# Kernel optimization log

Hardware: AMD Instinct MI355X
Metric: run time of the kernel (lower is better)

## Reference

```python
import jax, jax.numpy as jnp
import numpy as np

B, S, D, E, K, F = 2, 1024, 1024, 8, 2, 2048


def setup_inputs() -> dict:
    key = jax.random.key(0)
    k0, k1, k2, k3 = jax.random.split(key, 4)
    x = jax.random.normal(k0, (B, S, D), dtype=jnp.float32)
    gate_w = (jax.random.normal(k1, (E, D), dtype=jnp.float32) * 0.02)  # nn.init.normal_(std=0.02)
    # nn.Linear default init ~ U(-1/sqrt(fan_in), 1/sqrt(fan_in)); use same scale
    w1 = jax.random.uniform(k2, (E, F, D), dtype=jnp.float32, minval=-1.0, maxval=1.0) / np.float32(np.sqrt(D))
    w2 = jax.random.uniform(k3, (E, D, F), dtype=jnp.float32, minval=-1.0, maxval=1.0) / np.float32(np.sqrt(F))
    norm_w = jnp.ones((D,), dtype=jnp.float32)
    scale = jnp.full((1,), -4.0, dtype=jnp.float32)
    return {"x": x, "gate_w": gate_w, "w1": w1, "w2": w2, "norm_w": norm_w, "scale": scale}


def reference(x, gate_w, w1, w2, norm_w, scale):
    b, s, d = x.shape
    e = gate_w.shape[0]
    t = b * s
    eps = jnp.finfo(x.dtype).eps  # torch RMSNorm eps=None -> dtype eps
    # RMSNorm
    xn = x * jax.lax.rsqrt(jnp.mean(x * x, axis=-1, keepdims=True) + eps) * norm_w
    xf = xn.reshape(t, d)
    # router
    logits = xf @ gate_w.T                       # [T, E]
    prob = jax.nn.softmax(logits, axis=-1)
    topk_w, topk_e = jax.lax.top_k(prob, K)      # [T, K]
    topk_w = topk_w / jnp.clip(jnp.sum(topk_w, axis=-1, keepdims=True), 1e-6)
    # dense combine weights [T, E]: sum of slot weights routed to each expert
    combine = jnp.sum(jax.nn.one_hot(topk_e, e, dtype=xf.dtype) * topk_w[..., None], axis=1)
    # all-expert FFN, weighted combine (same math as the gather/index_add loop)
    h = jax.nn.silu(jnp.einsum('td,efd->tef', xf, w1))   # [T, E, F]
    out = jnp.einsum('tef,edf,te->td', h, w2, combine)    # [T, D]
    # load-balance aux loss (Switch eq.4), f_e from top-1 slot, detached
    f_e = jnp.mean(jax.nn.one_hot(topk_e[:, 0], e, dtype=prob.dtype), axis=0)
    lb_loss = e * jnp.sum(jax.lax.stop_gradient(f_e) * jnp.mean(prob, axis=0))
    sc = jax.nn.sigmoid(scale)[0]
    return (x + sc * out.reshape(b, s, d), lb_loss)
```

## Files before the change

kernel.cpp:

```cpp
#include <hip/hip_runtime.h>
#include <stdint.h>

#define T_TOK 2048
#define DD 1024
#define EE 8
#define FF 2048
#define NSLOT 4096
#define SLOTPAD 4224
#define CVT_BLOCKS 6144

typedef __attribute__((ext_vector_type(8))) __bf16 bf16x8;
typedef __attribute__((ext_vector_type(4))) float floatx4;

__device__ __forceinline__ unsigned short f2bf(float f){
  union { float f; unsigned u; } v; v.f = f;
  unsigned r = v.u + 0x7fffu + ((v.u >> 16) & 1u);
  return (unsigned short)(r >> 16);
}

__global__ __launch_bounds__(256) void k_front(
    const float* __restrict__ x, const float* __restrict__ gw,
    const float* __restrict__ nw,
    const float* __restrict__ w1, const float* __restrict__ w2,
    unsigned short* __restrict__ xn,
    int* __restrict__ topk_id, float* __restrict__ topk_w,
    float* __restrict__ probbuf,
    unsigned short* __restrict__ w1b, unsigned short* __restrict__ w2b)
{
  const int tid = threadIdx.x;
  if (blockIdx.x >= T_TOK){
    const int n4 = EE * FF * DD / 4;
    int i = (blockIdx.x - T_TOK) * 256 + tid;
    const int stride = CVT_BLOCKS * 256;
    for (; i < 2 * n4; i += stride){
      const int j = (i < n4) ? i : i - n4;
      const float4 v = (i < n4) ? ((const float4*)w1)[j] : ((const float4*)w2)[j];
      ushort4 o; o.x = f2bf(v.x); o.y = f2bf(v.y); o.z = f2bf(v.z); o.w = f2bf(v.w);
      if (i < n4) ((ushort4*)w1b)[j] = o; else ((ushort4*)w2b)[j] = o;
    }
    return;
  }
  const int t = blockIdx.x;
  const float4 xv = ((const float4*)(x + (size_t)t * DD))[tid];
  float ss = xv.x*xv.x + xv.y*xv.y + xv.z*xv.z + xv.w*xv.w;
  #pragma unroll
  for (int o = 32; o > 0; o >>= 1) ss += __shfl_down(ss, o);
  __shared__ float s_ss[4];
  __shared__ float s_p[4][8];
  if ((tid & 63) == 0) s_ss[tid >> 6] = ss;
  __syncthreads();
  const float tot = s_ss[0] + s_ss[1] + s_ss[2] + s_ss[3];
  const float inv = rsqrtf(tot * (1.0f / DD) + 1.1920929e-7f);
  const float4 nv = ((const float4*)nw)[tid];
  float4 xnv;
  xnv.x = xv.x*inv*nv.x; xnv.y = xv.y*inv*nv.y;
  xnv.z = xv.z*inv*nv.z; xnv.w = xv.w*inv*nv.w;
  ushort4 bv; bv.x = f2bf(xnv.x); bv.y = f2bf(xnv.y); bv.z = f2bf(xnv.z); bv.w = f2bf(xnv.w);
  ((ushort4*)(xn + (size_t)t * DD))[tid] = bv;
  float p[8];
  #pragma unroll
  for (int e = 0; e < 8; e++){
    const float4 g = ((const float4*)(gw + e * DD))[tid];
    p[e] = xnv.x*g.x + xnv.y*g.y + xnv.z*g.z + xnv.w*g.w;
  }
  #pragma unroll
  for (int e = 0; e < 8; e++){
    #pragma unroll
    for (int o = 32; o > 0; o >>= 1) p[e] += __shfl_down(p[e], o);
  }
  if ((tid & 63) == 0){
    #pragma unroll
    for (int e = 0; e < 8; e++) s_p[tid >> 6][e] = p[e];
  }
  __syncthreads();
  if (tid == 0){
    float lg[8], pr[8];
    #pragma unroll
    for (int e = 0; e < 8; e++) lg[e] = s_p[0][e] + s_p[1][e] + s_p[2][e] + s_p[3][e];
    float mx = lg[0];
    for (int e = 1; e < 8; e++) mx = fmaxf(mx, lg[e]);
    float sum = 0.f;
    for (int e = 0; e < 8; e++){ pr[e] = __expf(lg[e] - mx); sum += pr[e]; }
    const float is = 1.f / sum;
    for (int e = 0; e < 8; e++) pr[e] *= is;
    #pragma unroll
    for (int e = 0; e < 8; e++) probbuf[t * 8 + e] = pr[e];
    int e1 = 0;
    for (int e = 1; e < 8; e++) if (pr[e] > pr[e1]) e1 = e;
    int e2 = (e1 == 0) ? 1 : 0;
    for (int e = 0; e < 8; e++) if (e != e1 && e != e2 && pr[e] > pr[e2]) e2 = e;
    const float wsum = fmaxf(pr[e1] + pr[e2], 1e-6f);
    topk_id[2*t] = e1; topk_id[2*t+1] = e2;
    topk_w[2*t] = pr[e1] / wsum; topk_w[2*t+1] = pr[e2] / wsum;
  }
}

__global__ __launch_bounds__(256) void k_stats(
    const int* __restrict__ topk_id, const float* __restrict__ topk_w,
    const float* __restrict__ probbuf,
    int* __restrict__ counts, int* __restrict__ bases,
    int* __restrict__ slots_of, int* __restrict__ tok_of,
    float* __restrict__ slot_w,
    float* __restrict__ lb_out)
{
  const int tid = threadIdx.x;
  __shared__ int s_scan[256][8];
  __shared__ int s_base[8];

  int ids[16];
  int lc[8] = {}, lc1[8] = {};
  float lsp[8] = {};
  #pragma unroll
  for (int j = 0; j < 8; j++){
    const int t = tid * 8 + j;
    const int e1 = topk_id[2*t], e2 = topk_id[2*t+1];
    ids[2*j] = e1; ids[2*j+1] = e2;
    lc[e1]++; lc[e2]++; lc1[e1]++;
    const float4 p0 = ((const float4*)(probbuf + t * 8))[0];
    const float4 p1 = ((const float4*)(probbuf + t * 8))[1];
    lsp[0] += p0.x; lsp[1] += p0.y; lsp[2] += p0.z; lsp[3] += p0.w;
    lsp[4] += p1.x; lsp[5] += p1.y; lsp[6] += p1.z; lsp[7] += p1.w;
  }
  #pragma unroll
  for (int e = 0; e < 8; e++) s_scan[tid][e] = lc[e];
  __syncthreads();
  for (int off = 1; off < 256; off <<= 1){
    int v[8];
    if (tid >= off){
      #pragma unroll
      for (int e = 0; e < 8; e++) v[e] = s_scan[tid - off][e];
    }
    __syncthreads();
    if (tid >= off){
      #pragma unroll
      for (int e = 0; e < 8; e++) s_scan[tid][e] += v[e];
    }
    __syncthreads();
  }
  int   rc1[8]; float rsp[8];
  #pragma unroll
  for (int e = 0; e < 8; e++){ rc1[e] = lc1[e]; rsp[e] = lsp[e]; }
  #pragma unroll
  for (int e = 0; e < 8; e++){
    #pragma unroll
    for (int o = 32; o > 0; o >>= 1){
      rc1[e] += __shfl_down(rc1[e], o);
      rsp[e] += __shfl_down(rsp[e], o);
    }
  }
  __shared__ int   s_c1[4][8];
  __shared__ float s_sp[4][8];
  if ((tid & 63) == 0){
    const int w = tid >> 6;
    #pragma unroll
    for (int e = 0; e < 8; e++){ s_c1[w][e] = rc1[e]; s_sp[w][e] = rsp[e]; }
  }
  __syncthreads();
  if (tid == 0){
    int b = 0; float lb = 0.f;
    for (int e = 0; e < 8; e++){
      const int tot = s_scan[255][e];
      counts[e] = tot; bases[e] = b; s_base[e] = b; b += tot;
      const int   c1 = s_c1[0][e] + s_c1[1][e] + s_c1[2][e] + s_c1[3][e];
      const float sp = s_sp[0][e] + s_sp[1][e] + s_sp[2][e] + s_sp[3][e];
      lb += (float)c1 * sp;
    }
    lb_out[0] = 8.f * lb * (1.f / ((float)T_TOK * (float)T_TOK));
  }
  __syncthreads();
  int rank[8];
  #pragma unroll
  for (int e = 0; e < 8; e++) rank[e] = s_scan[tid][e] - lc[e];
  #pragma unroll
  for (int j = 0; j < 8; j++){
    const int t = tid * 8 + j;
    #pragma unroll
    for (int k = 0; k < 2; k++){
      const int e = ids[2*j + k];
      const int slot = s_base[e] + rank[e]++;
      slots_of[2*t + k] = slot;
      tok_of[slot] = t;
      slot_w[slot] = topk_w[2*t + k];
    }
  }
}

template<int KDIM, int NDIM, int MODE>
__global__ __launch_bounds__(256) void k_gemm(
    const unsigned short* __restrict__ Ag,
    const unsigned short* __restrict__ Bw,
    const int* __restrict__ counts, const int* __restrict__ bases,
    const int* __restrict__ tok_of,
    const float* __restrict__ slot_w,
    void* __restrict__ Cout)
{
  constexpr int NT = NDIM / 128;
  const int e  = blockIdx.x & 7;
  const int g  = blockIdx.x >> 3;
  const int mt = g / NT;
  const int nt = g - mt * NT;
  const int M = counts[e];
  if (mt * 128 >= M) return;
  const int sbase = bases[e];

  __shared__ __align__(16) unsigned short As[128 * 32];
  __shared__ __align__(16) unsigned short Bs[128 * 32];

  const int tid = threadIdx.x;
  const int l = tid & 63;
  const int w = tid >> 6;
  const int wm = (w >> 1) * 64, wn = (w & 1) * 64;
  const int lrow = l & 15, lq = l >> 4;

  const unsigned short* arow[2];
  int kcs[2];
  #pragma unroll
  for (int i = 0; i < 2; i++){
    const int c = tid + i * 256;
    const int row = c >> 2, q = c & 3;
    kcs[i] = ((q - (row >> 1)) & 3) * 8;
    if (MODE == 0){
      const int slot = min(sbase + mt * 128 + row, NSLOT - 1);
      arow[i] = Ag + (size_t)tok_of[slot] * KDIM;
    } else {
      arow[i] = Ag + (size_t)(sbase + mt * 128 + row) * KDIM;
    }
  }
  const unsigned short* B0 = Bw + (size_t)e * NDIM * KDIM + (size_t)(nt * 128) * KDIM;

  floatx4 acc[4][4] = {};

  for (int k0 = 0; k0 < KDIM; k0 += 32){
    #pragma unroll
    for (int i = 0; i < 2; i++){
      const int c = tid + i * 256;
      const int row = c >> 2;
      const unsigned short* ga = arow[i] + k0 + kcs[i];
      const unsigned short* gb = B0 + (size_t)row * KDIM + k0 + kcs[i];
      __builtin_amdgcn_global_load_lds(
          (__attribute__((address_space(1))) unsigned int*)ga,
          (__attribute__((address_space(3))) unsigned int*)(As + c * 8), 16, 0, 0);
      __builtin_amdgcn_global_load_lds(
          (__attribute__((address_space(1))) unsigned int*)gb,
          (__attribute__((address_space(3))) unsigned int*)(Bs + c * 8), 16, 0, 0);
    }
    __syncthreads();
    bf16x8 af[4], bfv[4];
    #pragma unroll
    for (int mi = 0; mi < 4; mi++){
      const int row = wm + mi * 16 + lrow;
      const int p = (lq + (row >> 1)) & 3;
      af[mi] = *(const bf16x8*)(As + row * 32 + p * 8);
    }
    #pragma unroll
    for (int ni = 0; ni < 4; ni++){
      const int row = wn + ni * 16 + lrow;
      const int p = (lq + (row >> 1)) & 3;
      bfv[ni] = *(const bf16x8*)(Bs + row * 32 + p * 8);
    }
    #pragma unroll
    for (int mi = 0; mi < 4; mi++)
      #pragma unroll
      for (int ni = 0; ni < 4; ni++)
        acc[mi][ni] = __builtin_amdgcn_mfma_f32_16x16x32_bf16(af[mi], bfv[ni], acc[mi][ni], 0, 0, 0);
    __syncthreads();
  }

  const int rb = lq * 4;
  #pragma unroll
  for (int mi = 0; mi < 4; mi++){
    #pragma unroll
    for (int r = 0; r < 4; r++){
      const int row = mt * 128 + wm + mi * 16 + rb + r;
      if (row < M){
        #pragma unroll
        for (int ni = 0; ni < 4; ni++){
          const int col = nt * 128 + wn + ni * 16 + (l & 15);
          const float v = acc[mi][ni][r];
          if (MODE == 0){
            const float s = v / (1.f + __expf(-v));
            ((unsigned short*)Cout)[(size_t)(sbase + row) * NDIM + col] = f2bf(s);
          } else {
            const float wgt = slot_w[sbase + row];
            ((float*)Cout)[(size_t)(sbase + row) * NDIM + col] = v * wgt;
          }
        }
      }
    }
  }
}

__global__ __launch_bounds__(256) void k_combine(
    const float* __restrict__ x, const float* __restrict__ Og,
    const int* __restrict__ slots_of, const float* __restrict__ scale,
    float* __restrict__ out)
{
  const int i = blockIdx.x * 256 + threadIdx.x;
  const int t = i >> 8;
  const int j = i & 255;
  const int s0 = slots_of[2*t], s1 = slots_of[2*t+1];
  const float4 a = ((const float4*)(Og + (size_t)s0 * DD))[j];
  const float4 b = ((const float4*)(Og + (size_t)s1 * DD))[j];
  const float4 xv = ((const float4*)x)[i];
  const float sc = 1.f / (1.f + __expf(-scale[0]));
  float4 o;
  o.x = xv.x + sc * (a.x + b.x);
  o.y = xv.y + sc * (a.y + b.y);
  o.z = xv.z + sc * (a.z + b.z);
  o.w = xv.w + sc * (a.w + b.w);
  ((float4*)out)[i] = o;
}

extern "C" void kernel_launch(void* const* d_in, const int* in_sizes, int n_in,
                              void* d_out, int out_size, void* d_ws, size_t ws_size,
                              hipStream_t stream)
{
  const float* x     = (const float*)d_in[0];
  const float* gw    = (const float*)d_in[1];
  const float* w1    = (const float*)d_in[2];
  const float* w2    = (const float*)d_in[3];
  const float* nw    = (const float*)d_in[4];
  const float* scale = (const float*)d_in[5];
  float* out = (float*)d_out;

  char* ws = (char*)d_ws;
  int*   counts  = (int*)(ws + 0);
  int*   bases   = (int*)(ws + 64);
  int*   topk_id = (int*)(ws + 1024);
  float* topk_w  = (float*)(ws + 20480);
  int*   slots_of= (int*)(ws + 40960);
  float* slot_w  = (float*)(ws + 61440);
  int*   tok_of  = (int*)(ws + 81920);
  float* probbuf = (float*)(ws + 102400);
  unsigned short* xn  = (unsigned short*)(ws + 262144);
  unsigned short* Hg  = xn + (size_t)T_TOK * DD;
  float*          Og  = (float*)(Hg + (size_t)SLOTPAD * FF);
  unsigned short* w1b = (unsigned short*)(Og + (size_t)SLOTPAD * DD);
  unsigned short* w2b = w1b + (size_t)EE * FF * DD;

  k_front<<<T_TOK + CVT_BLOCKS, 256, 0, stream>>>(x, gw, nw, w1, w2, xn,
                                                  topk_id, topk_w, probbuf, w1b, w2b);
  k_stats<<<1, 256, 0, stream>>>(topk_id, topk_w, probbuf, counts, bases,
                                 slots_of, tok_of, slot_w, out + (size_t)T_TOK * DD);
  k_gemm<1024, 2048, 0><<<EE * 16 * (FF/128), 256, 0, stream>>>(xn, w1b, counts, bases, tok_of, nullptr, Hg);
  k_gemm<2048, 1024, 1><<<EE * 16 * (DD/128), 256, 0, stream>>>(Hg, w2b, counts, bases, nullptr, slot_w, Og);
  k_combine<<<T_TOK * DD / 4 / 256, 256, 0, stream>>>(x, Og, slots_of, scale, out);
}
```

Before: 274.5 us.

## Convert fp32 expert weights to bf16 inside GEMM loads instead of separate pass

Drops the separate weight-conversion pass over both fp32 expert weight tensors. The GEMMs now read fp32 weights directly, convert them to bf16 in registers and store them to LDS, which removes a full write and re-read of the bf16 weight copies. The second GEMM's output is also stored as bf16, halving the combine kernel's traffic, and the grid order is changed so M-tiles vary fastest for weight reuse in cache. The trade-off is twice the global bytes per weight tile inside the GEMM, synchronous register-path loads instead of direct-to-LDS loads, and lower output precision.

```diff
diff --git a/kernel.cpp b/kernel.cpp
--- a/kernel.cpp
+++ b/kernel.cpp
@@ -7,40 +7,28 @@
 #define FF 2048
 #define NSLOT 4096
 #define SLOTPAD 4224
-#define CVT_BLOCKS 6144
 
 typedef __attribute__((ext_vector_type(8))) __bf16 bf16x8;
 typedef __attribute__((ext_vector_type(4))) float floatx4;
+typedef __attribute__((ext_vector_type(8))) unsigned short ushort8;
 
 __device__ __forceinline__ unsigned short f2bf(float f){
   union { float f; unsigned u; } v; v.f = f;
   unsigned r = v.u + 0x7fffu + ((v.u >> 16) & 1u);
   return (unsigned short)(r >> 16);
 }
-
-__global__ __launch_bounds__(256) void k_front(
+__device__ __forceinline__ float bf2f(unsigned short h){
+  union { unsigned u; float f; } v; v.u = (unsigned)h << 16; return v.f;
+}
+
+__global__ __launch_bounds__(256) void k_rms_router(
     const float* __restrict__ x, const float* __restrict__ gw,
     const float* __restrict__ nw,
-    const float* __restrict__ w1, const float* __restrict__ w2,
     unsigned short* __restrict__ xn,
     int* __restrict__ topk_id, float* __restrict__ topk_w,
-    float* __restrict__ probbuf,
-    unsigned short* __restrict__ w1b, unsigned short* __restrict__ w2b)
-{
-  const int tid = threadIdx.x;
-  if (blockIdx.x >= T_TOK){
-    const int n4 = EE * FF * DD / 4;
-    int i = (blockIdx.x - T_TOK) * 256 + tid;
-    const int stride = CVT_BLOCKS * 256;
-    for (; i < 2 * n4; i += stride){
-      const int j = (i < n4) ? i : i - n4;
-      const float4 v = (i < n4) ? ((const float4*)w1)[j] : ((const float4*)w2)[j];
-      ushort4 o; o.x = f2bf(v.x); o.y = f2bf(v.y); o.z = f2bf(v.z); o.w = f2bf(v.w);
-      if (i < n4) ((ushort4*)w1b)[j] = o; else ((ushort4*)w2b)[j] = o;
-    }
-    return;
-  }
-  const int t = blockIdx.x;
+    float* __restrict__ probbuf)
+{
+  const int t = blockIdx.x, tid = threadIdx.x;
   const float4 xv = ((const float4*)(x + (size_t)t * DD))[tid];
   float ss = xv.x*xv.x + xv.y*xv.y + xv.z*xv.z + xv.w*xv.w;
   #pragma unroll
@@ -188,17 +176,17 @@
 template<int KDIM, int NDIM, int MODE>
 __global__ __launch_bounds__(256) void k_gemm(
     const unsigned short* __restrict__ Ag,
-    const unsigned short* __restrict__ Bw,
+    const float* __restrict__ Bw,
     const int* __restrict__ counts, const int* __restrict__ bases,
     const int* __restrict__ tok_of,
     const float* __restrict__ slot_w,
-    void* __restrict__ Cout)
+    unsigned short* __restrict__ Cout)
 {
   constexpr int NT = NDIM / 128;
   const int e  = blockIdx.x & 7;
   const int g  = blockIdx.x >> 3;
-  const int mt = g / NT;
-  const int nt = g - mt * NT;
+  const int nt = g / 16;
+  const int mt = g - nt * 16;
   const int M = counts[e];
   if (mt * 128 >= M) return;
   const int sbase = bases[e];
@@ -213,20 +201,21 @@
   const int lrow = l & 15, lq = l >> 4;
 
   const unsigned short* arow[2];
+  const float* brow[2];
   int kcs[2];
   #pragma unroll
   for (int i = 0; i < 2; i++){
     const int c = tid + i * 256;
     const int row = c >> 2, q = c & 3;
     kcs[i] = ((q - (row >> 1)) & 3) * 8;
+    const int vrow = min(mt * 128 + row, M - 1);
     if (MODE == 0){
-      const int slot = min(sbase + mt * 128 + row, NSLOT - 1);
-      arow[i] = Ag + (size_t)tok_of[slot] * KDIM;
+      arow[i] = Ag + (size_t)tok_of[sbase + vrow] * KDIM;
     } else {
-      arow[i] = Ag + (size_t)(sbase + mt * 128 + row) * KDIM;
-    }
-  }
-  const unsigned short* B0 = Bw + (size_t)e * NDIM * KDIM + (size_t)(nt * 128) * KDIM;
+      arow[i] = Ag + (size_t)(sbase + vrow) * KDIM;
+    }
+    brow[i] = Bw + (size_t)e * NDIM * KDIM + (size_t)(nt * 128 + row) * KDIM + kcs[i];
+  }
 
   floatx4 acc[4][4] = {};
 
@@ -234,15 +223,18 @@
     #pragma unroll
     for (int i = 0; i < 2; i++){
       const int c = tid + i * 256;
-      const int row = c >> 2;
-      const unsigned short* ga = arow[i] + k0 + kcs[i];
-      const unsigned short* gb = B0 + (size_t)row * KDIM + k0 + kcs[i];
       __builtin_amdgcn_global_load_lds(
-          (__attribute__((address_space(1))) unsigned int*)ga,
+          (__attribute__((address_space(1))) unsigned int*)(arow[i] + k0 + kcs[i]),
           (__attribute__((address_space(3))) unsigned int*)(As + c * 8), 16, 0, 0);
-      __builtin_amdgcn_global_load_lds(
-          (__attribute__((address_space(1))) unsigned int*)gb,
-          (__attribute__((address_space(3))) unsigned int*)(Bs + c * 8), 16, 0, 0);
+    }
+    #pragma unroll
+    for (int i = 0; i < 2; i++){
+      const float4* p = (const float4*)(brow[i] + k0);
+      const float4 b0 = p[0], b1 = p[1];
+      ushort8 o;
+      o[0] = f2bf(b0.x); o[1] = f2bf(b0.y); o[2] = f2bf(b0.z); o[3] = f2bf(b0.w);
+      o[4] = f2bf(b1.x); o[5] = f2bf(b1.y); o[6] = f2bf(b1.z); o[7] = f2bf(b1.w);
+      *(ushort8*)(Bs + (size_t)(tid + i * 256) * 8) = o;
     }
     __syncthreads();
     bf16x8 af[4], bfv[4];
@@ -279,10 +271,10 @@
           const float v = acc[mi][ni][r];
           if (MODE == 0){
             const float s = v / (1.f + __expf(-v));
-            ((unsigned short*)Cout)[(size_t)(sbase + row) * NDIM + col] = f2bf(s);
+            Cout[(size_t)(sbase + row) * NDIM + col] = f2bf(s);
           } else {
             const float wgt = slot_w[sbase + row];
-            ((float*)Cout)[(size_t)(sbase + row) * NDIM + col] = v * wgt;
+            Cout[(size_t)(sbase + row) * NDIM + col] = f2bf(v * wgt);
           }
         }
       }
@@ -291,24 +283,30 @@
 }
 
 __global__ __launch_bounds__(256) void k_combine(
-    const float* __restrict__ x, const float* __restrict__ Og,
+    const float* __restrict__ x, const unsigned short* __restrict__ Og,
     const int* __restrict__ slots_of, const float* __restrict__ scale,
     float* __restrict__ out)
 {
   const int i = blockIdx.x * 256 + threadIdx.x;
-  const int t = i >> 8;
-  const int j = i & 255;
+  const int t = i >> 7;
+  const int j = i & 127;
   const int s0 = slots_of[2*t], s1 = slots_of[2*t+1];
-  const float4 a = ((const float4*)(Og + (size_t)s0 * DD))[j];
-  const float4 b = ((const float4*)(Og + (size_t)s1 * DD))[j];
-  const float4 xv = ((const float4*)x)[i];
+  const ushort8 a = ((const ushort8*)(Og + (size_t)s0 * DD))[j];
+  const ushort8 b = ((const ushort8*)(Og + (size_t)s1 * DD))[j];
+  const float4 x0 = ((const float4*)(x + (size_t)t * DD))[2*j];
+  const float4 x1 = ((const float4*)(x + (size_t)t * DD))[2*j + 1];
   const float sc = 1.f / (1.f + __expf(-scale[0]));
-  float4 o;
-  o.x = xv.x + sc * (a.x + b.x);
-  o.y = xv.y + sc * (a.y + b.y);
-  o.z = xv.z + sc * (a.z + b.z);
-  o.w = xv.w + sc * (a.w + b.w);
-  ((float4*)out)[i] = o;
+  float4 o0, o1;
+  o0.x = x0.x + sc * (bf2f(a[0]) + bf2f(b[0]));
+  o0.y = x0.y + sc * (bf2f(a[1]) + bf2f(b[1]));
+  o0.z = x0.z + sc * (bf2f(a[2]) + bf2f(b[2]));
+  o0.w = x0.w + sc * (bf2f(a[3]) + bf2f(b[3]));
+  o1.x = x1.x + sc * (bf2f(a[4]) + bf2f(b[4]));
+  o1.y = x1.y + sc * (bf2f(a[5]) + bf2f(b[5]));
+  o1.z = x1.z + sc * (bf2f(a[6]) + bf2f(b[6]));
+  o1.w = x1.w + sc * (bf2f(a[7]) + bf2f(b[7]));
+  ((float4*)(out + (size_t)t * DD))[2*j] = o0;
+  ((float4*)(out + (size_t)t * DD))[2*j + 1] = o1;
 }
 
 extern "C" void kernel_launch(void* const* d_in, const int* in_sizes, int n_in,
@@ -334,15 +332,12 @@
   float* probbuf = (float*)(ws + 102400);
   unsigned short* xn  = (unsigned short*)(ws + 262144);
   unsigned short* Hg  = xn + (size_t)T_TOK * DD;
-  float*          Og  = (float*)(Hg + (size_t)SLOTPAD * FF);
-  unsigned short* w1b = (unsigned short*)(Og + (size_t)SLOTPAD * DD);
-  unsigned short* w2b = w1b + (size_t)EE * FF * DD;
-
-  k_front<<<T_TOK + CVT_BLOCKS, 256, 0, stream>>>(x, gw, nw, w1, w2, xn,
-                                                  topk_id, topk_w, probbuf, w1b, w2b);
+  unsigned short* Og  = Hg + (size_t)SLOTPAD * FF;
+
+  k_rms_router<<<T_TOK, 256, 0, stream>>>(x, gw, nw, xn, topk_id, topk_w, probbuf);
   k_stats<<<1, 256, 0, stream>>>(topk_id, topk_w, probbuf, counts, bases,
                                  slots_of, tok_of, slot_w, out + (size_t)T_TOK * DD);
-  k_gemm<1024, 2048, 0><<<EE * 16 * (FF/128), 256, 0, stream>>>(xn, w1b, counts, bases, tok_of, nullptr, Hg);
-  k_gemm<2048, 1024, 1><<<EE * 16 * (DD/128), 256, 0, stream>>>(Hg, w2b, counts, bases, nullptr, slot_w, Og);
-  k_combine<<<T_TOK * DD / 4 / 256, 256, 0, stream>>>(x, Og, slots_of, scale, out);
-}
+  k_gemm<1024, 2048, 0><<<EE * 16 * (FF/128), 256, 0, stream>>>(xn, w1, counts, bases, tok_of, nullptr, Hg);
+  k_gemm<2048, 1024, 1><<<EE * 16 * (DD/128), 256, 0, stream>>>(Hg, w2, counts, bases, nullptr, slot_w, Og);
+  k_combine<<<T_TOK * DD / 8 / 256, 256, 0, stream>>>(x, Og, slots_of, scale, out);
+}
```

Result: slower. 352.9 us (+28.6%).
